# Optimization experiments

Hardware: AMD Instinct MI355X
Metric: run time of the kernel (lower is better)

## Reference

```python
import jax, jax.numpy as jnp
import numpy as np

IN_F = 8192
OUT_F = 8192
R = 16
LORA_ALPHA = 32
BLOCK = 64
SCALING = LORA_ALPHA / R  # 2.0
NUMEL = IN_F * OUT_F


def dequantize_4bit(packed, scales):
    # packed: [numel//2] bytes (stored as int32 in [0,255]); element 2i = low nibble, 2i+1 = high nibble
    low = packed & 0xF
    high = (packed >> 4) & 0xF
    q = jnp.stack([low, high], axis=-1).reshape(-1)          # [numel] ints in [0,15]
    flat = q.astype(jnp.float32) - 8.0                        # signed 4-bit
    flat = (flat.reshape(-1, BLOCK) * scales[:, None]).reshape(-1)  # blockwise scale
    return flat.reshape(OUT_F, IN_F)


def setup_inputs() -> dict:
    key = jax.random.key(0)
    k1, k2, k3, k4, k5 = jax.random.split(key, 5)
    x = jax.random.normal(k1, (1, 64, IN_F), dtype=jnp.float32)
    packed_weights = jax.random.randint(k2, (NUMEL // 2,), 0, 256, dtype=jnp.int32)
    block_scales = jax.random.uniform(k3, (NUMEL // BLOCK,), dtype=jnp.float32) * 0.05
    # kaiming_uniform(a=sqrt(5)) on [R, IN_F] -> bound = 1/sqrt(IN_F)
    bound = 1.0 / np.sqrt(IN_F)
    lora_A = jax.random.uniform(k4, (R, IN_F), minval=-bound, maxval=bound, dtype=jnp.float32)
    # original init is zeros; use small randn for a non-trivial baseline
    lora_B = jax.random.normal(k5, (OUT_F, R), dtype=jnp.float32) * 0.02
    return {"x": x, "packed_weights": packed_weights, "block_scales": block_scales,
            "lora_A": lora_A, "lora_B": lora_B}


def reference(x, packed_weights, block_scales, lora_A, lora_B):
    W = dequantize_4bit(packed_weights, block_scales).astype(x.dtype)  # [OUT_F, IN_F]
    base_out = jnp.einsum('bsi,oi->bso', x, W)                         # no bias (bias_buffer=None)
    lora_out = jnp.einsum('bsr,or->bso', jnp.einsum('bsi,ri->bsr', x, lora_A), lora_B) * SCALING
    return base_out + lora_out
```

## Files before the change

kernel.cpp:

```cpp
#include <hip/hip_runtime.h>
#include <hip/hip_bf16.h>

#define IN_F 8192
#define OUT_F 8192
#define SEQ 64
#define LORA_R 16
#define KH 4096

typedef __attribute__((ext_vector_type(4))) float f32x4;
typedef __attribute__((ext_vector_type(4))) int i32x4;
typedef __attribute__((ext_vector_type(8))) unsigned short u16x8;
typedef __attribute__((ext_vector_type(4))) unsigned short u16x4;
typedef _Float16 f16x2 __attribute__((ext_vector_type(2)));
typedef _Float16 f16x8 __attribute__((ext_vector_type(8)));

__global__ __launch_bounds__(512) void k_prep(
    const float* __restrict__ x, const float* __restrict__ A,
    unsigned short* __restrict__ xb, float* __restrict__ t,
    float* __restrict__ out) {
    const int tid = threadIdx.x;
    const int gi = blockIdx.x * 512 + tid;

    f32x4 v = *(const f32x4*)(x + gi * 4);
    u16x4 h;
    h[0] = __builtin_bit_cast(unsigned short, (_Float16)v.x);
    h[1] = __builtin_bit_cast(unsigned short, (_Float16)v.y);
    h[2] = __builtin_bit_cast(unsigned short, (_Float16)v.z);
    h[3] = __builtin_bit_cast(unsigned short, (_Float16)v.w);
    *(u16x4*)(xb + gi * 4) = h;
    *(f32x4*)(out + gi * 4) = (f32x4){0.f, 0.f, 0.f, 0.f};

    if (blockIdx.x < SEQ) {
        __shared__ float p[LORA_R][33];
        const int s = blockIdx.x;
        const int r = tid & 15, seg = tid >> 4;
        const float* xr = x + s * IN_F + seg * 256;
        const float* ar = A + r * IN_F + seg * 256;
        float acc = 0.f;
        #pragma unroll 8
        for (int j = 0; j < 64; ++j) {
            f32x4 xv = *(const f32x4*)(xr + j * 4);
            f32x4 av = *(const f32x4*)(ar + j * 4);
            acc = fmaf(xv.x, av.x, acc);
            acc = fmaf(xv.y, av.y, acc);
            acc = fmaf(xv.z, av.z, acc);
            acc = fmaf(xv.w, av.w, acc);
        }
        p[r][seg] = acc;
        __syncthreads();
        if (tid < LORA_R) {
            float sum = 0.f;
            #pragma unroll
            for (int g = 0; g < 32; ++g) sum += p[tid][g];
            t[s * LORA_R + tid] = sum;
        }
    }
}

__global__ __launch_bounds__(512, 4) void k_main(
    const int* __restrict__ packed, const float* __restrict__ scales,
    const unsigned short* __restrict__ xb, const float* __restrict__ t,
    const float* __restrict__ B, float* __restrict__ out) {
    __shared__ char lds[60928];
    _Float16* xs = (_Float16*)lds;
    int* wt = (int*)(lds + 34816);
    float* scs = (float*)(lds + 52224);
    float* accs = (float*)lds;

    const int tid = threadIdx.x;
    const int n0 = (blockIdx.x >> 1) * 32;
    const int kh = blockIdx.x & 1;
    const int w = tid >> 6, lane = tid & 63;
    const int nh = w >> 2, wkk = w & 3;
    const int q = lane >> 4, c16 = lane & 15;

    {
        int row = tid >> 4, g = tid & 15;
        f32x4 v = *(const f32x4*)(scales + (n0 + row) * (IN_F / 64) + kh * 64 + g * 4);
        *(f32x4*)(scs + row * 68 + g * 4) = v;
    }

    const int xrow = tid >> 3, xseg = tid & 7;
    const int wrow = tid >> 4, wg = tid & 15;
    const unsigned short* xsrc = xb + xrow * IN_F + kh * KH + xseg * 16;
    const int* wsrc = packed + (long)(n0 + wrow) * (IN_F / 2) + kh * (KH / 2) + wg * 4;
    _Float16* xdst0 = xs + xrow * 136 + xseg * 16;
    int* wdst0 = wt + wrow * 68 + wg * 4;

    f32x4 acc[4];
    #pragma unroll
    for (int mt = 0; mt < 4; ++mt) acc[mt] = (f32x4){0.f, 0.f, 0.f, 0.f};

    const f16x2 c1032 = {(_Float16)1032.0f, (_Float16)1032.0f};

    {
        u16x8 a0 = *(const u16x8*)(xsrc);
        u16x8 b0 = *(const u16x8*)(xsrc + 8);
        i32x4 w0 = __builtin_nontemporal_load((const i32x4*)wsrc);
        *(u16x8*)xdst0 = a0;
        *(u16x8*)(xdst0 + 8) = b0;
        *(i32x4*)wdst0 = w0;
    }
    __syncthreads();

    for (int kt = 0; kt < 32; ++kt) {
        const int cur = kt & 1;
        u16x8 ga, gb; i32x4 gw;
        if (kt < 31) {
            ga = *(const u16x8*)(xsrc + (kt + 1) * 128);
            gb = *(const u16x8*)(xsrc + (kt + 1) * 128 + 8);
            gw = __builtin_nontemporal_load((const i32x4*)(wsrc + (kt + 1) * 64));
        }
        i32x4 pv = *(const i32x4*)(wt + cur * (32 * 68) + (nh * 16 + c16) * 68 + wkk * 16 + q * 4);
        float scf = scs[(nh * 16 + c16) * 68 + kt * 2 + (wkk >> 1)];
        _Float16 sch = (_Float16)scf;
        f16x2 sc2 = {sch, sch};
        f16x8 bf;
        #pragma unroll
        for (int m = 0; m < 4; ++m) {
            unsigned u = ((((unsigned)pv[m] << 12) | (unsigned)pv[m]) & 0x000F000Fu) | 0x64006400u;
            f16x2 hh = __builtin_bit_cast(f16x2, u);
            hh = (hh - c1032) * sc2;
            bf[2 * m] = hh.x;
            bf[2 * m + 1] = hh.y;
        }
        const _Float16* xbase = xs + cur * (64 * 136) + wkk * 32 + q * 8;
        #pragma unroll
        for (int mt = 0; mt < 4; ++mt) {
            f16x8 af = *(const f16x8*)(xbase + (mt * 16 + c16) * 136);
            acc[mt] = __builtin_amdgcn_mfma_f32_16x16x32_f16(af, bf, acc[mt], 0, 0, 0);
        }
        __syncthreads();
        if (kt < 31) {
            *(u16x8*)(xs + (1 - cur) * (64 * 136) + xrow * 136 + xseg * 16)     = ga;
            *(u16x8*)(xs + (1 - cur) * (64 * 136) + xrow * 136 + xseg * 16 + 8) = gb;
            *(i32x4*)(wt + (1 - cur) * (32 * 68) + wrow * 68 + wg * 4)          = gw;
        }
        __syncthreads();
    }

    float* myacc = accs + w * (64 * 17);
    #pragma unroll
    for (int mt = 0; mt < 4; ++mt)
        #pragma unroll
        for (int r = 0; r < 4; ++r)
            myacc[(mt * 16 + q * 4 + r) * 17 + c16] = acc[mt][r];
    __syncthreads();

    #pragma unroll
    for (int j = 0; j < 4; ++j) {
        int p = tid + j * 512;
        int s = p >> 5, c = p & 31;
        const float* ab = accs + (c >> 4) * 4 * (64 * 17) + s * 17 + (c & 15);
        float v = ab[0] + ab[64 * 17] + ab[2 * 64 * 17] + ab[3 * 64 * 17];
        if (kh == 0) {
            const float* tp = t + s * LORA_R;
            const float* bp = B + (n0 + c) * LORA_R;
            float lr = 0.f;
            #pragma unroll
            for (int r = 0; r < LORA_R; ++r) lr = fmaf(tp[r], bp[r], lr);
            v += 2.0f * lr;
        }
        unsafeAtomicAdd(&out[s * OUT_F + n0 + c], v);
    }
}

extern "C" void kernel_launch(void* const* d_in, const int* in_sizes, int n_in,
                              void* d_out, int out_size, void* d_ws, size_t ws_size,
                              hipStream_t stream) {
    const float* x      = (const float*)d_in[0];
    const int* packed   = (const int*)d_in[1];
    const float* scales = (const float*)d_in[2];
    const float* lora_A = (const float*)d_in[3];
    const float* lora_B = (const float*)d_in[4];
    float* out = (float*)d_out;

    unsigned short* xb = (unsigned short*)d_ws;
    float* t = (float*)((char*)d_ws + (size_t)SEQ * IN_F * 2);

    k_prep<<<256, 512, 0, stream>>>(x, lora_A, xb, t, out);
    k_main<<<512, 512, 0, stream>>>(packed, scales, xb, t, lora_B, out);
}
```

Baseline: 234.9 us.

## Pre-swizzle x and scales into MFMA fragment order and drop LDS staging

The prep kernel now writes x as fp16 in MFMA fragment order and transposes the block scales into a per-tile layout. The main kernel then loads operands straight from global memory into registers with a two-deep software prefetch, so the shared-memory double buffer and its two barriers per k-step go away. The split-K factor goes from 2 to 4, and each wave covers both 16-column halves. The aim is to remove LDS traffic and synchronisation from a memory-bound weight stream, at the cost of more atomics, an extra scale-transpose pass, and x being re-read from L2 by each block.

```diff
diff --git a/kernel.cpp b/kernel.cpp
--- a/kernel.cpp
+++ b/kernel.cpp
@@ -5,40 +5,58 @@
 #define OUT_F 8192
 #define SEQ 64
 #define LORA_R 16
-#define KH 4096
 
 typedef __attribute__((ext_vector_type(4))) float f32x4;
 typedef __attribute__((ext_vector_type(4))) int i32x4;
 typedef __attribute__((ext_vector_type(8))) unsigned short u16x8;
-typedef __attribute__((ext_vector_type(4))) unsigned short u16x4;
 typedef _Float16 f16x2 __attribute__((ext_vector_type(2)));
 typedef _Float16 f16x8 __attribute__((ext_vector_type(8)));
 
-__global__ __launch_bounds__(512) void k_prep(
+__global__ __launch_bounds__(256) void k_prep(
     const float* __restrict__ x, const float* __restrict__ A,
-    unsigned short* __restrict__ xb, float* __restrict__ t,
-    float* __restrict__ out) {
-    const int tid = threadIdx.x;
-    const int gi = blockIdx.x * 512 + tid;
-
-    f32x4 v = *(const f32x4*)(x + gi * 4);
-    u16x4 h;
-    h[0] = __builtin_bit_cast(unsigned short, (_Float16)v.x);
-    h[1] = __builtin_bit_cast(unsigned short, (_Float16)v.y);
-    h[2] = __builtin_bit_cast(unsigned short, (_Float16)v.z);
-    h[3] = __builtin_bit_cast(unsigned short, (_Float16)v.w);
-    *(u16x4*)(xb + gi * 4) = h;
-    *(f32x4*)(out + gi * 4) = (f32x4){0.f, 0.f, 0.f, 0.f};
-
-    if (blockIdx.x < SEQ) {
-        __shared__ float p[LORA_R][33];
-        const int s = blockIdx.x;
+    const float* __restrict__ scales,
+    unsigned short* __restrict__ x_sw, float* __restrict__ sc_sw,
+    float* __restrict__ t, float* __restrict__ out) {
+    const int bid = blockIdx.x, tid = threadIdx.x;
+    if (bid < 256) {
+        int g = bid * 256 + tid;
+        int c16 = g & 15, q = (g >> 4) & 3, mt = (g >> 6) & 3, kstep = g >> 8;
+        int row = mt * 16 + c16, k0 = kstep * 32 + q * 8;
+        const float* src = x + row * IN_F + k0;
+        f32x4 v0 = *(const f32x4*)src;
+        f32x4 v1 = *(const f32x4*)(src + 4);
+        u16x8 h;
+        h[0] = __builtin_bit_cast(unsigned short, (_Float16)v0.x);
+        h[1] = __builtin_bit_cast(unsigned short, (_Float16)v0.y);
+        h[2] = __builtin_bit_cast(unsigned short, (_Float16)v0.z);
+        h[3] = __builtin_bit_cast(unsigned short, (_Float16)v0.w);
+        h[4] = __builtin_bit_cast(unsigned short, (_Float16)v1.x);
+        h[5] = __builtin_bit_cast(unsigned short, (_Float16)v1.y);
+        h[6] = __builtin_bit_cast(unsigned short, (_Float16)v1.z);
+        h[7] = __builtin_bit_cast(unsigned short, (_Float16)v1.w);
+        *(u16x8*)(x_sw + g * 8) = h;
+    } else if (bid < 768) {
+        int i = (bid - 256) * 256 + tid;
+        *(f32x4*)(out + i * 4) = (f32x4){0.f, 0.f, 0.f, 0.f};
+    } else if (bid < 1792) {
+        int e0 = ((bid - 768) * 256 + tid) * 4;
+        int c16 = e0 & 15, nh = (e0 >> 4) & 1, kblk = (e0 >> 5) & 127, ntile = e0 >> 12;
+        int rowb = ntile * 32 + nh * 16 + c16;
+        f32x4 v;
+        v.x = scales[(rowb + 0) * 128 + kblk];
+        v.y = scales[(rowb + 1) * 128 + kblk];
+        v.z = scales[(rowb + 2) * 128 + kblk];
+        v.w = scales[(rowb + 3) * 128 + kblk];
+        *(f32x4*)(sc_sw + e0) = v;
+    } else {
+        __shared__ float p[LORA_R][17];
+        const int s = bid - 1792;
         const int r = tid & 15, seg = tid >> 4;
-        const float* xr = x + s * IN_F + seg * 256;
-        const float* ar = A + r * IN_F + seg * 256;
+        const float* xr = x + s * IN_F + seg * 512;
+        const float* ar = A + r * IN_F + seg * 512;
         float acc = 0.f;
         #pragma unroll 8
-        for (int j = 0; j < 64; ++j) {
+        for (int j = 0; j < 128; ++j) {
             f32x4 xv = *(const f32x4*)(xr + j * 4);
             f32x4 av = *(const f32x4*)(ar + j * 4);
             acc = fmaf(xv.x, av.x, acc);
@@ -51,117 +69,104 @@
         if (tid < LORA_R) {
             float sum = 0.f;
             #pragma unroll
-            for (int g = 0; g < 32; ++g) sum += p[tid][g];
+            for (int g = 0; g < 16; ++g) sum += p[tid][g];
             t[s * LORA_R + tid] = sum;
         }
     }
 }
 
-__global__ __launch_bounds__(512, 4) void k_main(
-    const int* __restrict__ packed, const float* __restrict__ scales,
-    const unsigned short* __restrict__ xb, const float* __restrict__ t,
+__global__ __launch_bounds__(256, 4) void k_main(
+    const int* __restrict__ packed, const unsigned short* __restrict__ x_sw,
+    const float* __restrict__ sc_sw, const float* __restrict__ t,
     const float* __restrict__ B, float* __restrict__ out) {
-    __shared__ char lds[60928];
-    _Float16* xs = (_Float16*)lds;
-    int* wt = (int*)(lds + 34816);
-    float* scs = (float*)(lds + 52224);
-    float* accs = (float*)lds;
+    __shared__ float accs[4][64][33];
 
     const int tid = threadIdx.x;
-    const int n0 = (blockIdx.x >> 1) * 32;
-    const int kh = blockIdx.x & 1;
+    const int ntile = blockIdx.x >> 2, kq = blockIdx.x & 3;
     const int w = tid >> 6, lane = tid & 63;
-    const int nh = w >> 2, wkk = w & 3;
     const int q = lane >> 4, c16 = lane & 15;
+    const int ksg0 = kq * 64 + w * 16;
 
-    {
-        int row = tid >> 4, g = tid & 15;
-        f32x4 v = *(const f32x4*)(scales + (n0 + row) * (IN_F / 64) + kh * 64 + g * 4);
-        *(f32x4*)(scs + row * 68 + g * 4) = v;
-    }
+    const unsigned short* xp = x_sw + ((ksg0 * 16 + q) * 16 + c16) * 8;
+    const int* wp = packed + (ntile * 32 + c16) * 4096 + ksg0 * 16 + q * 4;
+    const float* scp = sc_sw + (ntile * 128) * 32 + c16;
 
-    const int xrow = tid >> 3, xseg = tid & 7;
-    const int wrow = tid >> 4, wg = tid & 15;
-    const unsigned short* xsrc = xb + xrow * IN_F + kh * KH + xseg * 16;
-    const int* wsrc = packed + (long)(n0 + wrow) * (IN_F / 2) + kh * (KH / 2) + wg * 4;
-    _Float16* xdst0 = xs + xrow * 136 + xseg * 16;
-    int* wdst0 = wt + wrow * 68 + wg * 4;
+    f32x4 acc[8];
+    #pragma unroll
+    for (int i = 0; i < 8; ++i) acc[i] = (f32x4){0.f, 0.f, 0.f, 0.f};
 
-    f32x4 acc[4];
-    #pragma unroll
-    for (int mt = 0; mt < 4; ++mt) acc[mt] = (f32x4){0.f, 0.f, 0.f, 0.f};
+    f16x8 xf[2][4];
+    i32x4 wv[2][2];
+    float sc[2][2];
+
+    auto loadstep = [&](int s, int set) {
+        #pragma unroll
+        for (int mt = 0; mt < 4; ++mt)
+            xf[set][mt] = *(const f16x8*)(xp + s * 2048 + mt * 512);
+        wv[set][0] = *(const i32x4*)(wp + s * 16);
+        wv[set][1] = *(const i32x4*)(wp + 16 * 4096 + s * 16);
+        int kb = (ksg0 + s) >> 1;
+        sc[set][0] = scp[(kb * 2 + 0) * 16];
+        sc[set][1] = scp[(kb * 2 + 1) * 16];
+    };
+
+    loadstep(0, 0);
+    loadstep(1, 1);
 
     const f16x2 c1032 = {(_Float16)1032.0f, (_Float16)1032.0f};
 
-    {
-        u16x8 a0 = *(const u16x8*)(xsrc);
-        u16x8 b0 = *(const u16x8*)(xsrc + 8);
-        i32x4 w0 = __builtin_nontemporal_load((const i32x4*)wsrc);
-        *(u16x8*)xdst0 = a0;
-        *(u16x8*)(xdst0 + 8) = b0;
-        *(i32x4*)wdst0 = w0;
-    }
-    __syncthreads();
+    #pragma unroll
+    for (int s = 0; s < 16; ++s) {
+        const int cur = s & 1;
+        f16x8 a0 = xf[cur][0], a1 = xf[cur][1], a2 = xf[cur][2], a3 = xf[cur][3];
+        i32x4 w0 = wv[cur][0], w1 = wv[cur][1];
+        float s0 = sc[cur][0], s1 = sc[cur][1];
+        if (s + 2 < 16) loadstep(s + 2, cur);
 
-    for (int kt = 0; kt < 32; ++kt) {
-        const int cur = kt & 1;
-        u16x8 ga, gb; i32x4 gw;
-        if (kt < 31) {
-            ga = *(const u16x8*)(xsrc + (kt + 1) * 128);
-            gb = *(const u16x8*)(xsrc + (kt + 1) * 128 + 8);
-            gw = __builtin_nontemporal_load((const i32x4*)(wsrc + (kt + 1) * 64));
+        #pragma unroll
+        for (int nh = 0; nh < 2; ++nh) {
+            i32x4 pv = nh ? w1 : w0;
+            _Float16 sch = (_Float16)(nh ? s1 : s0);
+            f16x2 sc2 = {sch, sch};
+            f16x8 bf;
+            #pragma unroll
+            for (int m = 0; m < 4; ++m) {
+                unsigned u = ((((unsigned)pv[m] << 12) | (unsigned)pv[m]) & 0x000F000Fu) | 0x64006400u;
+                f16x2 hh = __builtin_bit_cast(f16x2, u);
+                hh = (hh - c1032) * sc2;
+                bf[2 * m] = hh.x;
+                bf[2 * m + 1] = hh.y;
+            }
+            acc[nh * 4 + 0] = __builtin_amdgcn_mfma_f32_16x16x32_f16(a0, bf, acc[nh * 4 + 0], 0, 0, 0);
+            acc[nh * 4 + 1] = __builtin_amdgcn_mfma_f32_16x16x32_f16(a1, bf, acc[nh * 4 + 1], 0, 0, 0);
+            acc[nh * 4 + 2] = __builtin_amdgcn_mfma_f32_16x16x32_f16(a2, bf, acc[nh * 4 + 2], 0, 0, 0);
+            acc[nh * 4 + 3] = __builtin_amdgcn_mfma_f32_16x16x32_f16(a3, bf, acc[nh * 4 + 3], 0, 0, 0);
         }
-        i32x4 pv = *(const i32x4*)(wt + cur * (32 * 68) + (nh * 16 + c16) * 68 + wkk * 16 + q * 4);
-        float scf = scs[(nh * 16 + c16) * 68 + kt * 2 + (wkk >> 1)];
-        _Float16 sch = (_Float16)scf;
-        f16x2 sc2 = {sch, sch};
-        f16x8 bf;
-        #pragma unroll
-        for (int m = 0; m < 4; ++m) {
-            unsigned u = ((((unsigned)pv[m] << 12) | (unsigned)pv[m]) & 0x000F000Fu) | 0x64006400u;
-            f16x2 hh = __builtin_bit_cast(f16x2, u);
-            hh = (hh - c1032) * sc2;
-            bf[2 * m] = hh.x;
-            bf[2 * m + 1] = hh.y;
-        }
-        const _Float16* xbase = xs + cur * (64 * 136) + wkk * 32 + q * 8;
-        #pragma unroll
-        for (int mt = 0; mt < 4; ++mt) {
-            f16x8 af = *(const f16x8*)(xbase + (mt * 16 + c16) * 136);
-            acc[mt] = __builtin_amdgcn_mfma_f32_16x16x32_f16(af, bf, acc[mt], 0, 0, 0);
-        }
-        __syncthreads();
-        if (kt < 31) {
-            *(u16x8*)(xs + (1 - cur) * (64 * 136) + xrow * 136 + xseg * 16)     = ga;
-            *(u16x8*)(xs + (1 - cur) * (64 * 136) + xrow * 136 + xseg * 16 + 8) = gb;
-            *(i32x4*)(wt + (1 - cur) * (32 * 68) + wrow * 68 + wg * 4)          = gw;
-        }
-        __syncthreads();
     }
 
-    float* myacc = accs + w * (64 * 17);
     #pragma unroll
-    for (int mt = 0; mt < 4; ++mt)
+    for (int nh = 0; nh < 2; ++nh)
         #pragma unroll
-        for (int r = 0; r < 4; ++r)
-            myacc[(mt * 16 + q * 4 + r) * 17 + c16] = acc[mt][r];
+        for (int mt = 0; mt < 4; ++mt)
+            #pragma unroll
+            for (int r = 0; r < 4; ++r)
+                accs[w][mt * 16 + q * 4 + r][nh * 16 + c16] = acc[nh * 4 + mt][r];
     __syncthreads();
 
     #pragma unroll
-    for (int j = 0; j < 4; ++j) {
-        int p = tid + j * 512;
+    for (int j = 0; j < 8; ++j) {
+        int p = tid + j * 256;
         int s = p >> 5, c = p & 31;
-        const float* ab = accs + (c >> 4) * 4 * (64 * 17) + s * 17 + (c & 15);
-        float v = ab[0] + ab[64 * 17] + ab[2 * 64 * 17] + ab[3 * 64 * 17];
-        if (kh == 0) {
+        float v = accs[0][s][c] + accs[1][s][c] + accs[2][s][c] + accs[3][s][c];
+        if (kq == 0) {
             const float* tp = t + s * LORA_R;
-            const float* bp = B + (n0 + c) * LORA_R;
+            const float* bp = B + (ntile * 32 + c) * LORA_R;
             float lr = 0.f;
             #pragma unroll
             for (int r = 0; r < LORA_R; ++r) lr = fmaf(tp[r], bp[r], lr);
             v += 2.0f * lr;
         }
-        unsafeAtomicAdd(&out[s * OUT_F + n0 + c], v);
+        unsafeAtomicAdd(&out[s * OUT_F + ntile * 32 + c], v);
     }
 }
 
@@ -175,9 +180,10 @@
     const float* lora_B = (const float*)d_in[4];
     float* out = (float*)d_out;
 
-    unsigned short* xb = (unsigned short*)d_ws;
-    float* t = (float*)((char*)d_ws + (size_t)SEQ * IN_F * 2);
+    unsigned short* x_sw = (unsigned short*)d_ws;
+    float* sc_sw = (float*)((char*)d_ws + (size_t)SEQ * IN_F * 2);
+    float* t = (float*)((char*)d_ws + (size_t)SEQ * IN_F * 2 + (size_t)OUT_F * 128 * 4);
 
-    k_prep<<<256, 512, 0, stream>>>(x, lora_A, xb, t, out);
-    k_main<<<512, 512, 0, stream>>>(packed, scales, xb, t, lora_B, out);
+    k_prep<<<1856, 256, 0, stream>>>(x, lora_A, scales, x_sw, sc_sw, t, out);
+    k_main<<<1024, 256, 0, stream>>>(packed, x_sw, sc_sw, t, lora_B, out);
 }
```

Result: slower. 261.8 us (+11.4%).

## Widen N tile to 64 with four-way K split and reuse x fragments

Applied to the files above, without the earlier changes.

Each block now covers 64 output columns over a quarter of K, and each warp computes two 16-column tiles that share the same loaded x fragments. This halves LDS reads of x per MFMA and gives each loop iteration more independent MFMA work. The double-buffered loop drops from two barriers per step to one, and weight loads no longer use the nontemporal hint. In exchange, LDS use grows, the epilogue runs in two phases, and the number of atomic partial sums written to the output doubles.

```diff
diff --git a/kernel.cpp b/kernel.cpp
--- a/kernel.cpp
+++ b/kernel.cpp
@@ -5,7 +5,6 @@
 #define OUT_F 8192
 #define SEQ 64
 #define LORA_R 16
-#define KH 4096
 
 typedef __attribute__((ext_vector_type(4))) float f32x4;
 typedef __attribute__((ext_vector_type(4))) int i32x4;
@@ -61,107 +60,122 @@
     const int* __restrict__ packed, const float* __restrict__ scales,
     const unsigned short* __restrict__ xb, const float* __restrict__ t,
     const float* __restrict__ B, float* __restrict__ out) {
-    __shared__ char lds[60928];
+    __shared__ char lds[78848];
     _Float16* xs = (_Float16*)lds;
-    int* wt = (int*)(lds + 34816);
-    float* scs = (float*)(lds + 52224);
-    float* accs = (float*)lds;
+    int*      wt = (int*)(lds + 34816);
+    float*    scs = (float*)(lds + 69632);
+    float*    accs = (float*)lds;
 
     const int tid = threadIdx.x;
-    const int n0 = (blockIdx.x >> 1) * 32;
-    const int kh = blockIdx.x & 1;
+    const int ntile = blockIdx.x >> 2, kq = blockIdx.x & 3;
+    const int n0 = ntile * 64;
     const int w = tid >> 6, lane = tid & 63;
     const int nh = w >> 2, wkk = w & 3;
     const int q = lane >> 4, c16 = lane & 15;
 
     {
-        int row = tid >> 4, g = tid & 15;
-        f32x4 v = *(const f32x4*)(scales + (n0 + row) * (IN_F / 64) + kh * 64 + g * 4);
-        *(f32x4*)(scs + row * 68 + g * 4) = v;
+        int row = tid >> 3, g = tid & 7;
+        f32x4 v = *(const f32x4*)(scales + (n0 + row) * 128 + kq * 32 + g * 4);
+        *(f32x4*)(scs + row * 36 + g * 4) = v;
     }
 
-    const int xrow = tid >> 3, xseg = tid & 7;
-    const int wrow = tid >> 4, wg = tid & 15;
-    const unsigned short* xsrc = xb + xrow * IN_F + kh * KH + xseg * 16;
-    const int* wsrc = packed + (long)(n0 + wrow) * (IN_F / 2) + kh * (KH / 2) + wg * 4;
-    _Float16* xdst0 = xs + xrow * 136 + xseg * 16;
-    int* wdst0 = wt + wrow * 68 + wg * 4;
+    const int srow = tid >> 3, sseg = tid & 7;
+    const unsigned short* xsrc = xb + srow * IN_F + kq * 2048 + sseg * 16;
+    const int* wsrc = packed + (long)(n0 + srow) * 4096 + kq * 1024 + sseg * 8;
 
-    f32x4 acc[4];
+    f32x4 acc[8];
     #pragma unroll
-    for (int mt = 0; mt < 4; ++mt) acc[mt] = (f32x4){0.f, 0.f, 0.f, 0.f};
+    for (int i = 0; i < 8; ++i) acc[i] = (f32x4){0.f, 0.f, 0.f, 0.f};
+
+    {
+        u16x8 xa = *(const u16x8*)xsrc;
+        u16x8 xbv = *(const u16x8*)(xsrc + 8);
+        i32x4 wa = *(const i32x4*)wsrc;
+        i32x4 wb = *(const i32x4*)(wsrc + 4);
+        *(u16x8*)(xs + srow * 136 + sseg * 16)     = xa;
+        *(u16x8*)(xs + srow * 136 + sseg * 16 + 8) = xbv;
+        *(i32x4*)(wt + srow * 68 + sseg * 8)       = wa;
+        *(i32x4*)(wt + srow * 68 + sseg * 8 + 4)   = wb;
+    }
+    __syncthreads();
 
     const f16x2 c1032 = {(_Float16)1032.0f, (_Float16)1032.0f};
 
-    {
-        u16x8 a0 = *(const u16x8*)(xsrc);
-        u16x8 b0 = *(const u16x8*)(xsrc + 8);
-        i32x4 w0 = __builtin_nontemporal_load((const i32x4*)wsrc);
-        *(u16x8*)xdst0 = a0;
-        *(u16x8*)(xdst0 + 8) = b0;
-        *(i32x4*)wdst0 = w0;
-    }
-    __syncthreads();
+    for (int kt = 0; kt < 16; ++kt) {
+        const int cur = kt & 1;
+        u16x8 xa, xbv; i32x4 wa, wb;
+        if (kt < 15) {
+            xa  = *(const u16x8*)(xsrc + (kt + 1) * 128);
+            xbv = *(const u16x8*)(xsrc + (kt + 1) * 128 + 8);
+            wa  = *(const i32x4*)(wsrc + (kt + 1) * 64);
+            wb  = *(const i32x4*)(wsrc + (kt + 1) * 64 + 4);
+        }
 
-    for (int kt = 0; kt < 32; ++kt) {
-        const int cur = kt & 1;
-        u16x8 ga, gb; i32x4 gw;
-        if (kt < 31) {
-            ga = *(const u16x8*)(xsrc + (kt + 1) * 128);
-            gb = *(const u16x8*)(xsrc + (kt + 1) * 128 + 8);
-            gw = __builtin_nontemporal_load((const i32x4*)(wsrc + (kt + 1) * 64));
+        const _Float16* xbase = xs + cur * (64 * 136) + wkk * 32 + q * 8;
+        f16x8 af0 = *(const f16x8*)(xbase + (0 * 16 + c16) * 136);
+        f16x8 af1 = *(const f16x8*)(xbase + (1 * 16 + c16) * 136);
+        f16x8 af2 = *(const f16x8*)(xbase + (2 * 16 + c16) * 136);
+        f16x8 af3 = *(const f16x8*)(xbase + (3 * 16 + c16) * 136);
+        #pragma unroll
+        for (int ct = 0; ct < 2; ++ct) {
+            const int row = nh * 32 + ct * 16 + c16;
+            i32x4 pv = *(const i32x4*)(wt + cur * (64 * 68) + row * 68 + wkk * 16 + q * 4);
+            float scf = scs[row * 36 + kt * 2 + (wkk >> 1)];
+            _Float16 sch = (_Float16)scf;
+            f16x2 sc2 = {sch, sch};
+            f16x8 bf;
+            #pragma unroll
+            for (int m = 0; m < 4; ++m) {
+                unsigned u = ((((unsigned)pv[m] << 12) | (unsigned)pv[m]) & 0x000F000Fu) | 0x64006400u;
+                f16x2 hh = __builtin_bit_cast(f16x2, u);
+                hh = (hh - c1032) * sc2;
+                bf[2 * m] = hh.x;
+                bf[2 * m + 1] = hh.y;
+            }
+            acc[ct * 4 + 0] = __builtin_amdgcn_mfma_f32_16x16x32_f16(af0, bf, acc[ct * 4 + 0], 0, 0, 0);
+            acc[ct * 4 + 1] = __builtin_amdgcn_mfma_f32_16x16x32_f16(af1, bf, acc[ct * 4 + 1], 0, 0, 0);
+            acc[ct * 4 + 2] = __builtin_amdgcn_mfma_f32_16x16x32_f16(af2, bf, acc[ct * 4 + 2], 0, 0, 0);
+            acc[ct * 4 + 3] = __builtin_amdgcn_mfma_f32_16x16x32_f16(af3, bf, acc[ct * 4 + 3], 0, 0, 0);
         }
-        i32x4 pv = *(const i32x4*)(wt + cur * (32 * 68) + (nh * 16 + c16) * 68 + wkk * 16 + q * 4);
-        float scf = scs[(nh * 16 + c16) * 68 + kt * 2 + (wkk >> 1)];
-        _Float16 sch = (_Float16)scf;
-        f16x2 sc2 = {sch, sch};
-        f16x8 bf;
-        #pragma unroll
-        for (int m = 0; m < 4; ++m) {
-            unsigned u = ((((unsigned)pv[m] << 12) | (unsigned)pv[m]) & 0x000F000Fu) | 0x64006400u;
-            f16x2 hh = __builtin_bit_cast(f16x2, u);
-            hh = (hh - c1032) * sc2;
-            bf[2 * m] = hh.x;
-            bf[2 * m + 1] = hh.y;
-        }
-        const _Float16* xbase = xs + cur * (64 * 136) + wkk * 32 + q * 8;
-        #pragma unroll
-        for (int mt = 0; mt < 4; ++mt) {
-            f16x8 af = *(const f16x8*)(xbase + (mt * 16 + c16) * 136);
-            acc[mt] = __builtin_amdgcn_mfma_f32_16x16x32_f16(af, bf, acc[mt], 0, 0, 0);
-        }
-        __syncthreads();
-        if (kt < 31) {
-            *(u16x8*)(xs + (1 - cur) * (64 * 136) + xrow * 136 + xseg * 16)     = ga;
-            *(u16x8*)(xs + (1 - cur) * (64 * 136) + xrow * 136 + xseg * 16 + 8) = gb;
-            *(i32x4*)(wt + (1 - cur) * (32 * 68) + wrow * 68 + wg * 4)          = gw;
+        if (kt < 15) {
+            *(u16x8*)(xs + (1 - cur) * (64 * 136) + srow * 136 + sseg * 16)     = xa;
+            *(u16x8*)(xs + (1 - cur) * (64 * 136) + srow * 136 + sseg * 16 + 8) = xbv;
+            *(i32x4*)(wt + (1 - cur) * (64 * 68) + srow * 68 + sseg * 8)        = wa;
+            *(i32x4*)(wt + (1 - cur) * (64 * 68) + srow * 68 + sseg * 8 + 4)    = wb;
         }
         __syncthreads();
     }
 
-    float* myacc = accs + w * (64 * 17);
     #pragma unroll
-    for (int mt = 0; mt < 4; ++mt)
+    for (int ph = 0; ph < 2; ++ph) {
+        if (nh == ph) {
+            #pragma unroll
+            for (int ct = 0; ct < 2; ++ct)
+                #pragma unroll
+                for (int mt = 0; mt < 4; ++mt)
+                    #pragma unroll
+                    for (int r = 0; r < 4; ++r)
+                        accs[wkk * 2112 + (mt * 16 + q * 4 + r) * 33 + ct * 16 + c16] = acc[ct * 4 + mt][r];
+        }
+        __syncthreads();
         #pragma unroll
-        for (int r = 0; r < 4; ++r)
-            myacc[(mt * 16 + q * 4 + r) * 17 + c16] = acc[mt][r];
-    __syncthreads();
-
-    #pragma unroll
-    for (int j = 0; j < 4; ++j) {
-        int p = tid + j * 512;
-        int s = p >> 5, c = p & 31;
-        const float* ab = accs + (c >> 4) * 4 * (64 * 17) + s * 17 + (c & 15);
-        float v = ab[0] + ab[64 * 17] + ab[2 * 64 * 17] + ab[3 * 64 * 17];
-        if (kh == 0) {
-            const float* tp = t + s * LORA_R;
-            const float* bp = B + (n0 + c) * LORA_R;
-            float lr = 0.f;
-            #pragma unroll
-            for (int r = 0; r < LORA_R; ++r) lr = fmaf(tp[r], bp[r], lr);
-            v += 2.0f * lr;
+        for (int j = 0; j < 4; ++j) {
+            int p = tid + j * 512;
+            int m = p >> 5, c = p & 31;
+            float v = accs[0 * 2112 + m * 33 + c] + accs[1 * 2112 + m * 33 + c] +
+                      accs[2 * 2112 + m * 33 + c] + accs[3 * 2112 + m * 33 + c];
+            int col = n0 + ph * 32 + c;
+            if (kq == 0) {
+                const float* tp = t + m * LORA_R;
+                const float* bp = B + col * LORA_R;
+                float lr = 0.f;
+                #pragma unroll
+                for (int r = 0; r < LORA_R; ++r) lr = fmaf(tp[r], bp[r], lr);
+                v += 2.0f * lr;
+            }
+            unsafeAtomicAdd(&out[m * OUT_F + col], v);
         }
-        unsafeAtomicAdd(&out[s * OUT_F + n0 + c], v);
+        __syncthreads();
     }
 }
 
```

After: 246.1 us. +4.7%, slower.
